# Performance work log

Measured on AMD Instinct MI355X. Metric: run time of the kernel, lower is better.

Reference implementation:

```python
import jax, jax.numpy as jnp
import numpy as np
from jax import lax

SEQ, BATCH, IN, HID, LAYERS = 2048, 64, 256, 256, 2


def setup_inputs() -> dict:
    key = jax.random.key(0)
    ks = jax.random.split(key, 5)
    k = np.sqrt(1.0 / HID).astype(np.float32)  # torch uniform(-sqrt(1/hidden), sqrt(1/hidden))
    x = jax.random.normal(ks[0], (SEQ, BATCH, IN), dtype=jnp.float32)
    h_0 = jax.random.normal(ks[1], (LAYERS, BATCH, HID), dtype=jnp.float32)
    W = jax.random.uniform(ks[2], (LAYERS, HID, IN), minval=-k, maxval=k, dtype=jnp.float32)
    U = jax.random.uniform(ks[3], (LAYERS, HID, HID), minval=-k, maxval=k, dtype=jnp.float32)
    b = jax.random.uniform(ks[4], (LAYERS, HID), minval=-k, maxval=k, dtype=jnp.float32)
    return {"x": x, "h_0": h_0, "W": W, "U": U, "b": b}


def reference(x, h_0, W, U, b):
    # Each layer independently maps x[t] -> h[layer] (original code feeds x[t] to every layer).
    def step(h, x_t):
        # h: [L, B, H], x_t: [B, I]
        h_new = jnp.tanh(
            jnp.einsum('bi,lhi->lbh', x_t, W)
            + jnp.einsum('lbh,lgh->lbg', h, U)
            + b[:, None, :]
        )
        return h_new, h_new[-1]  # output collects last layer's state

    h_n, output = lax.scan(step, h_0, x)
    return output, h_n
```

## Files before the change

### kernel.cpp

```cpp
#include <hip/hip_runtime.h>
#include <math.h>

#define SEQ 2048
#define BATCH 64
#define INF 256
#define HID 256
#define NL 2

typedef __attribute__((ext_vector_type(2))) _Float16 half2_t;

__global__ __launch_bounds__(256) void xw_kernel(
    const float* __restrict__ x,
    const float* __restrict__ W,
    const float* __restrict__ bias,
    float* __restrict__ pre0,
    float* __restrict__ pre1)
{
    __shared__ float As[64][68];
    __shared__ float Bs[64][68];

    const int mb = blockIdx.x * 64;
    const int nb = blockIdx.y * 64;
    const int l  = nb >> 8;
    const int hb = nb & 255;

    const int tid = threadIdx.x;
    const int tx = tid & 15;
    const int ty = tid >> 4;

    const float* Wl = W + (size_t)l * HID * INF;

    float acc[4][4] = {};

    const int lrow = tid >> 4;
    const int lkq  = tid & 15;

    for (int kb = 0; kb < INF; kb += 64) {
        #pragma unroll
        for (int rr = 0; rr < 4; ++rr) {
            const int m = lrow + rr * 16;
            float4 va = *(const float4*)&x[(size_t)(mb + m) * INF + kb + lkq * 4];
            As[lkq*4 + 0][m] = va.x; As[lkq*4 + 1][m] = va.y;
            As[lkq*4 + 2][m] = va.z; As[lkq*4 + 3][m] = va.w;
            float4 vb = *(const float4*)&Wl[(size_t)(hb + m) * INF + kb + lkq * 4];
            Bs[lkq*4 + 0][m] = vb.x; Bs[lkq*4 + 1][m] = vb.y;
            Bs[lkq*4 + 2][m] = vb.z; Bs[lkq*4 + 3][m] = vb.w;
        }
        __syncthreads();

        #pragma unroll 8
        for (int k = 0; k < 64; ++k) {
            float4 a = *(const float4*)&As[k][ty * 4];
            float4 b = *(const float4*)&Bs[k][tx * 4];
            acc[0][0] = fmaf(a.x, b.x, acc[0][0]);
            acc[0][1] = fmaf(a.x, b.y, acc[0][1]);
            acc[0][2] = fmaf(a.x, b.z, acc[0][2]);
            acc[0][3] = fmaf(a.x, b.w, acc[0][3]);
            acc[1][0] = fmaf(a.y, b.x, acc[1][0]);
            acc[1][1] = fmaf(a.y, b.y, acc[1][1]);
            acc[1][2] = fmaf(a.y, b.z, acc[1][2]);
            acc[1][3] = fmaf(a.y, b.w, acc[1][3]);
            acc[2][0] = fmaf(a.z, b.x, acc[2][0]);
            acc[2][1] = fmaf(a.z, b.y, acc[2][1]);
            acc[2][2] = fmaf(a.z, b.z, acc[2][2]);
            acc[2][3] = fmaf(a.z, b.w, acc[2][3]);
            acc[3][0] = fmaf(a.w, b.x, acc[3][0]);
            acc[3][1] = fmaf(a.w, b.y, acc[3][1]);
            acc[3][2] = fmaf(a.w, b.z, acc[3][2]);
            acc[3][3] = fmaf(a.w, b.w, acc[3][3]);
        }
        __syncthreads();
    }

    float bv[4];
    #pragma unroll
    for (int j = 0; j < 4; ++j)
        bv[j] = bias[l * HID + hb + tx * 4 + j];

    float* dst = (l == 0) ? pre0 : pre1;
    #pragma unroll
    for (int i = 0; i < 4; ++i) {
        float4 o;
        o.x = acc[i][0] + bv[0];
        o.y = acc[i][1] + bv[1];
        o.z = acc[i][2] + bv[2];
        o.w = acc[i][3] + bv[3];
        *(float4*)&dst[(size_t)(mb + ty * 4 + i) * HID + hb + tx * 4] = o;
    }
}

__device__ __forceinline__ float tanh_fast(float x) {
    float xc = fminf(fmaxf(x, -12.0f), 12.0f);
    float e  = __expf(2.0f * xc);
    return __fdividef(e - 1.0f, e + 1.0f);
}

__device__ __forceinline__ float dot2(unsigned ua, unsigned ub, float c) {
#if __has_builtin(__builtin_amdgcn_fdot2)
    return __builtin_amdgcn_fdot2(__builtin_bit_cast(half2_t, ua),
                                  __builtin_bit_cast(half2_t, ub), c, false);
#else
    half2_t a = __builtin_bit_cast(half2_t, ua);
    half2_t b = __builtin_bit_cast(half2_t, ub);
    c = fmaf((float)a.x, (float)b.x, c);
    return fmaf((float)a.y, (float)b.y, c);
#endif
}

__device__ __forceinline__ unsigned pk16(float a, float b) {
#if __has_builtin(__builtin_amdgcn_cvt_pkrtz)
    return __builtin_bit_cast(unsigned, __builtin_amdgcn_cvt_pkrtz(a, b));
#else
    half2_t h; h.x = (_Float16)a; h.y = (_Float16)b;
    return __builtin_bit_cast(unsigned, h);
#endif
}

__global__ __launch_bounds__(512, 2) void rnn_kernel(
    const float* __restrict__ h0,
    const float* __restrict__ U,
    const float* pre0,
    const float* pre1,
    float* out,
    float* hn)
{
    __shared__ alignas(16) unsigned h16[2][128];

    const int l = blockIdx.x >> 6;
    const int b = blockIdx.x & 63;
    const int tid = threadIdx.x;
    const int g = tid >> 1;
    const int c = tid & 1;

    uint4 uu[16];
    const float* Urow = U + (size_t)l * HID * HID + (size_t)g * HID + c * 128;
    #pragma unroll
    for (int r = 0; r < 16; ++r) {
        float4 f0 = *(const float4*)&Urow[r * 8];
        float4 f1 = *(const float4*)&Urow[r * 8 + 4];
        uu[r].x = pk16(f0.x, f0.y);
        uu[r].y = pk16(f0.z, f0.w);
        uu[r].z = pk16(f1.x, f1.y);
        uu[r].w = pk16(f1.z, f1.w);
    }
    #pragma unroll
    for (int r = 0; r < 16; ++r)
        asm volatile("" : "+v"(uu[r].x), "+v"(uu[r].y), "+v"(uu[r].z), "+v"(uu[r].w));

    if (tid < 128) {
        const float* h0p = h0 + (size_t)l * BATCH * HID + (size_t)b * HID;
        h16[0][tid] = pk16(h0p[tid * 2], h0p[tid * 2 + 1]);
    }
    __syncthreads();

    const float* pre = (l == 0) ? pre0 : pre1;
    const size_t bh = (size_t)b * HID + g;

    float preCur = pre[bh];
    float v = 0.0f;
    int cur = 0;

    for (int t = 0; t < SEQ; ++t) {
        float preNext = (t + 1 < SEQ) ? pre[(size_t)(t + 1) * BATCH * HID + bh] : 0.0f;

        float a0 = 0.f, a1 = 0.f, a2 = 0.f, a3 = 0.f;
        const uint4* hc = (const uint4*)&h16[cur][c * 64];
        #pragma unroll
        for (int r = 0; r < 16; ++r) {
            uint4 w = hc[r];
            a0 = dot2(w.x, uu[r].x, a0);
            a1 = dot2(w.y, uu[r].y, a1);
            a2 = dot2(w.z, uu[r].z, a2);
            a3 = dot2(w.w, uu[r].w, a3);
        }
        float s = (a0 + a1) + (a2 + a3);
        s += __shfl_xor(s, 1);

        v = tanh_fast(s + preCur);

        float vp = __shfl_xor(v, 2);
        if (c == 0) {
            if ((g & 1) == 0)
                h16[cur ^ 1][g >> 1] = pk16(v, vp);
            if (l == 1)
                out[(size_t)t * BATCH * HID + bh] = v;
        }
        preCur = preNext;
        cur ^= 1;
        __syncthreads();
    }

    if (c == 0)
        hn[(size_t)l * BATCH * HID + bh] = v;
}

extern "C" void kernel_launch(void* const* d_in, const int* in_sizes, int n_in,
                              void* d_out, int out_size, void* d_ws, size_t ws_size,
                              hipStream_t stream) {
    const float* x  = (const float*)d_in[0];
    const float* h0 = (const float*)d_in[1];
    const float* W  = (const float*)d_in[2];
    const float* U  = (const float*)d_in[3];
    const float* bs = (const float*)d_in[4];

    float* out  = (float*)d_out;
    float* pre0 = (float*)d_ws;
    float* pre1 = out;
    float* hn   = out + (size_t)SEQ * BATCH * HID;

    dim3 gridA(SEQ * BATCH / 64, (NL * HID) / 64);
    xw_kernel<<<gridA, 256, 0, stream>>>(x, W, bs, pre0, pre1);

    rnn_kernel<<<NL * BATCH, 512, 0, stream>>>(h0, U, pre0, pre1, out, hn);
}
```

Before: 2.137 ms.

## Move recurrent weights from registers to swizzled LDS in RNN kernel

The fp16-packed U rows that each thread held in 64 VGPRs are now stored in 128 KB of dynamic shared memory, using an XOR swizzle across 16-byte slots to reduce bank conflicts. The hidden-state buffer is split into two padded halves so that the two lanes of a row pair read separate regions. This frees registers but adds 16 LDS vector loads per thread on every step of the serial recurrence. With 128 KB of LDS per block, only one block may fit per CU.

```diff
diff --git a/kernel.cpp b/kernel.cpp
--- a/kernel.cpp
+++ b/kernel.cpp
@@ -116,6 +116,8 @@
 #endif
 }
 
+#define U_LDS_BYTES (128 * 1024)
+
 __global__ __launch_bounds__(512, 2) void rnn_kernel(
     const float* __restrict__ h0,
     const float* __restrict__ U,
@@ -124,32 +126,33 @@
     float* out,
     float* hn)
 {
-    __shared__ alignas(16) unsigned h16[2][128];
+    extern __shared__ uint4 Ulds[];
+    __shared__ unsigned h16[2][2][68];
 
     const int l = blockIdx.x >> 6;
     const int b = blockIdx.x & 63;
     const int tid = threadIdx.x;
     const int g = tid >> 1;
     const int c = tid & 1;
-
-    uint4 uu[16];
+    const int s7 = tid & 7;
+
     const float* Urow = U + (size_t)l * HID * HID + (size_t)g * HID + c * 128;
+    uint4* myU = Ulds + tid * 16;
     #pragma unroll
     for (int r = 0; r < 16; ++r) {
         float4 f0 = *(const float4*)&Urow[r * 8];
         float4 f1 = *(const float4*)&Urow[r * 8 + 4];
-        uu[r].x = pk16(f0.x, f0.y);
-        uu[r].y = pk16(f0.z, f0.w);
-        uu[r].z = pk16(f1.x, f1.y);
-        uu[r].w = pk16(f1.z, f1.w);
-    }
-    #pragma unroll
-    for (int r = 0; r < 16; ++r)
-        asm volatile("" : "+v"(uu[r].x), "+v"(uu[r].y), "+v"(uu[r].z), "+v"(uu[r].w));
+        uint4 p;
+        p.x = pk16(f0.x, f0.y);
+        p.y = pk16(f0.z, f0.w);
+        p.z = pk16(f1.x, f1.y);
+        p.w = pk16(f1.z, f1.w);
+        myU[r ^ s7] = p;
+    }
 
     if (tid < 128) {
         const float* h0p = h0 + (size_t)l * BATCH * HID + (size_t)b * HID;
-        h16[0][tid] = pk16(h0p[tid * 2], h0p[tid * 2 + 1]);
+        h16[0][tid >> 6][tid & 63] = pk16(h0p[tid * 2], h0p[tid * 2 + 1]);
     }
     __syncthreads();
 
@@ -164,14 +167,15 @@
         float preNext = (t + 1 < SEQ) ? pre[(size_t)(t + 1) * BATCH * HID + bh] : 0.0f;
 
         float a0 = 0.f, a1 = 0.f, a2 = 0.f, a3 = 0.f;
-        const uint4* hc = (const uint4*)&h16[cur][c * 64];
+        const uint4* hc = (const uint4*)&h16[cur][c][0];
         #pragma unroll
         for (int r = 0; r < 16; ++r) {
-            uint4 w = hc[r];
-            a0 = dot2(w.x, uu[r].x, a0);
-            a1 = dot2(w.y, uu[r].y, a1);
-            a2 = dot2(w.z, uu[r].z, a2);
-            a3 = dot2(w.w, uu[r].w, a3);
+            uint4 w  = hc[r];
+            uint4 uu = myU[r ^ s7];
+            a0 = dot2(w.x, uu.x, a0);
+            a1 = dot2(w.y, uu.y, a1);
+            a2 = dot2(w.z, uu.z, a2);
+            a3 = dot2(w.w, uu.w, a3);
         }
         float s = (a0 + a1) + (a2 + a3);
         s += __shfl_xor(s, 1);
@@ -181,7 +185,7 @@
         float vp = __shfl_xor(v, 2);
         if (c == 0) {
             if ((g & 1) == 0)
-                h16[cur ^ 1][g >> 1] = pk16(v, vp);
+                h16[cur ^ 1][g >> 7][(g >> 1) & 63] = pk16(v, vp);
             if (l == 1)
                 out[(size_t)t * BATCH * HID + bh] = v;
         }
@@ -208,8 +212,16 @@
     float* pre1 = out;
     float* hn   = out + (size_t)SEQ * BATCH * HID;
 
+    static bool attr_done = false;
+    if (!attr_done) {
+        hipFuncSetAttribute((const void*)rnn_kernel,
+                            hipFuncAttributeMaxDynamicSharedMemorySize,
+                            U_LDS_BYTES);
+        attr_done = true;
+    }
+
     dim3 gridA(SEQ * BATCH / 64, (NL * HID) / 64);
     xw_kernel<<<gridA, 256, 0, stream>>>(x, W, bs, pre0, pre1);
 
-    rnn_kernel<<<NL * BATCH, 512, 0, stream>>>(h0, U, pre0, pre1, out, hn);
-}
+    rnn_kernel<<<NL * BATCH, 512, U_LDS_BYTES, stream>>>(h0, U, pre0, pre1, out, hn);
+}
```

Result: slower. 2.711 ms (+26.9%).
